# Performance work log

Hardware: AMD Instinct MI355X
Metric: run time of the kernel (lower is better)

## Reference

```python
import jax, jax.numpy as jnp
import numpy as np

EMB = 1024
HEADS = 16
HEAD_DIM = EMB // HEADS
FF = 4 * EMB


def _gelu_tanh(x):
    c = jnp.sqrt(jnp.asarray(2.0 / jnp.pi, x.dtype))
    return 0.5 * x * (1.0 + jnp.tanh(c * (x + 0.044715 * x ** 3)))


def _layernorm(x, scale, shift, eps=1e-5):
    mean = jnp.mean(x, axis=-1, keepdims=True)
    var = jnp.mean((x - mean) ** 2, axis=-1, keepdims=True)
    return scale * (x - mean) / jnp.sqrt(var + eps) + shift


def setup_inputs() -> dict:
    key = jax.random.key(0)
    ks = jax.random.split(key, 8)
    s = 0.02
    return {
        "x": jax.random.normal(ks[0], (2, 2048, EMB), jnp.float32),
        "w_q": jax.random.normal(ks[1], (EMB, EMB), jnp.float32) * s,
        "w_k": jax.random.normal(ks[2], (EMB, EMB), jnp.float32) * s,
        "w_v": jax.random.normal(ks[3], (EMB, EMB), jnp.float32) * s,
        "w_o": jax.random.normal(ks[4], (EMB, EMB), jnp.float32) * s,
        "b_o": jnp.zeros((EMB,), jnp.float32),
        "ln1_scale": jnp.ones((EMB,), jnp.float32),
        "ln1_shift": jnp.zeros((EMB,), jnp.float32),
        "ln2_scale": jnp.ones((EMB,), jnp.float32),
        "ln2_shift": jnp.zeros((EMB,), jnp.float32),
        "w_ff1": jax.random.normal(ks[5], (EMB, FF), jnp.float32) * s,
        "b_ff1": jnp.zeros((FF,), jnp.float32),
        "w_ff2": jax.random.normal(ks[6], (FF, EMB), jnp.float32) * s,
        "b_ff2": jnp.zeros((EMB,), jnp.float32),
    }


def _attention(x, w_q, w_k, w_v, w_o, b_o):
    b, n, _ = x.shape
    q = (x @ w_q).reshape(b, n, HEADS, HEAD_DIM).transpose(0, 2, 1, 3)  # bhnd
    k = (x @ w_k).reshape(b, n, HEADS, HEAD_DIM).transpose(0, 2, 1, 3)
    v = (x @ w_v).reshape(b, n, HEADS, HEAD_DIM).transpose(0, 2, 1, 3)
    scores = jnp.einsum("bhqd,bhkd->bhqk", q, k)
    causal = jnp.triu(jnp.ones((n, n), bool), k=1)
    scores = jnp.where(causal, -jnp.inf, scores)
    # original scales AFTER masking (-inf stays -inf)
    attn = jax.nn.softmax(scores / jnp.sqrt(jnp.asarray(HEAD_DIM, x.dtype)), axis=-1)
    ctx = jnp.einsum("bhqk,bhkd->bhqd", attn, v)
    ctx = ctx.transpose(0, 2, 1, 3).reshape(b, n, EMB)
    return ctx @ w_o + b_o


def reference(x, w_q, w_k, w_v, w_o, b_o, ln1_scale, ln1_shift,
              ln2_scale, ln2_shift, w_ff1, b_ff1, w_ff2, b_ff2):
    h = _layernorm(x, ln1_scale, ln1_shift)
    h = _attention(h, w_q, w_k, w_v, w_o, b_o)
    x = x + h  # dropout is identity at drop_rate=0 / eval
    h = _layernorm(x, ln2_scale, ln2_shift)
    h = _gelu_tanh(h @ w_ff1 + b_ff1) @ w_ff2 + b_ff2
    return x + h
```

## Files before the change

### kernel.cpp

```cpp
#include <hip/hip_runtime.h>
#include <math.h>

#define EMB 1024
#define HEADS 16
#define HD 64
#define FF_DIM 4096
#define SEQ 2048
#define BATCH 2
#define NTOK (BATCH * SEQ)

typedef __bf16 bf16x8 __attribute__((ext_vector_type(8)));
typedef float f32x4 __attribute__((ext_vector_type(4)));

__device__ __forceinline__ unsigned short f2bf(float f) {
    union { float f; unsigned int u; } v; v.f = f;
    unsigned int r = v.u + 0x7fff + ((v.u >> 16) & 1);
    return (unsigned short)(r >> 16);
}

__device__ __forceinline__ float gelu_f(float x) {
    const float A = 1.5957691216057308f;
    const float B = 0.07135481282989427f;
    float zz = x * (A + B * x * x);
    return x * __builtin_amdgcn_rcpf(1.f + __expf(-zz));
}

#define GLOAD_LDS16(g, l)                                                      \
    __builtin_amdgcn_global_load_lds(                                          \
        (const __attribute__((address_space(1))) void*)(g),                    \
        (__attribute__((address_space(3))) void*)(l), 16, 0, 0)

__global__ __launch_bounds__(256) void ln_kernel(const float* __restrict__ x,
                                                 const float* __restrict__ scale,
                                                 const float* __restrict__ shift,
                                                 unsigned short* __restrict__ out) {
    int row = blockIdx.x;
    const float* xr = x + (size_t)row * EMB;
    unsigned short* yr = out + (size_t)row * EMB;
    int t = threadIdx.x;

    float v[4];
    float s = 0.f, s2 = 0.f;
#pragma unroll
    for (int i = 0; i < 4; i++) {
        v[i] = xr[t + i * 256];
        s += v[i];
        s2 += v[i] * v[i];
    }
    for (int o = 32; o > 0; o >>= 1) {
        s += __shfl_down(s, o, 64);
        s2 += __shfl_down(s2, o, 64);
    }
    __shared__ float red[4], red2[4];
    int wave = t >> 6;
    if ((t & 63) == 0) { red[wave] = s; red2[wave] = s2; }
    __syncthreads();
    if (t == 0) {
        float a = 0.f, b = 0.f;
#pragma unroll
        for (int i = 0; i < 4; i++) { a += red[i]; b += red2[i]; }
        red[0] = a; red2[0] = b;
    }
    __syncthreads();
    float mean = red[0] * (1.f / EMB);
    float var = red2[0] * (1.f / EMB) - mean * mean;
    float rstd = rsqrtf(var + 1e-5f);
#pragma unroll
    for (int i = 0; i < 4; i++) {
        int c = t + i * 256;
        yr[c] = f2bf(scale[c] * (v[i] - mean) * rstd + shift[c]);
    }
}

__global__ __launch_bounds__(256) void transpose_cast6(
    const float* __restrict__ w0, const float* __restrict__ w1,
    const float* __restrict__ w2, const float* __restrict__ w3,
    const float* __restrict__ w4, const float* __restrict__ w5,
    unsigned short* __restrict__ o0, unsigned short* __restrict__ o1,
    unsigned short* __restrict__ o2, unsigned short* __restrict__ o3,
    unsigned short* __restrict__ o4, unsigned short* __restrict__ o5) {
    __shared__ float tile[64][65];
    int id = blockIdx.x;
    const float* src; unsigned short* dst; int K, N, lid;
    if (id < 256)       { src = w0; dst = o0; K = 1024; N = 1024; lid = id; }
    else if (id < 512)  { src = w1; dst = o1; K = 1024; N = 1024; lid = id - 256; }
    else if (id < 768)  { src = w2; dst = o2; K = 1024; N = 1024; lid = id - 512; }
    else if (id < 1024) { src = w3; dst = o3; K = 1024; N = 1024; lid = id - 768; }
    else if (id < 2048) { src = w4; dst = o4; K = 1024; N = 4096; lid = id - 1024; }
    else                { src = w5; dst = o5; K = 4096; N = 1024; lid = id - 2048; }
    int tn = N >> 6;
    int k0 = (lid / tn) << 6, n0 = (lid % tn) << 6;
    int t = threadIdx.x;
    int rr = t >> 6, cc = t & 63;
#pragma unroll
    for (int i = 0; i < 16; i++) {
        int r = i * 4 + rr;
        tile[r][cc] = src[(size_t)(k0 + r) * N + n0 + cc];
    }
    __syncthreads();
#pragma unroll
    for (int i = 0; i < 16; i++) {
        int r = i * 4 + rr;
        dst[(size_t)(n0 + r) * K + k0 + cc] = f2bf(tile[cc][r]);
    }
}

template <int EPI>
__global__ __launch_bounds__(256) void mfma_gemm(
    const unsigned short* __restrict__ A,
    const unsigned short* __restrict__ Bt,
    void* __restrict__ Cv,
    const float* __restrict__ bias,
    const float* __restrict__ resid,
    int M, int N, int K) {
    __shared__ unsigned short As[128 * 32];
    __shared__ unsigned short Bs[128 * 32];

    const int t = threadIdx.x;
    const int w = t >> 6, lane = t & 63;
    const int m0 = blockIdx.y * 128, n0 = blockIdx.x * 128;

    const int sr0 = (w << 5) + (lane >> 2);
    const int sr1 = sr0 + 16;
    const int p = lane & 3;
    const int c0 = p ^ ((sr0 >> 1) & 3);
    const int c1 = p ^ ((sr1 >> 1) & 3);
    const unsigned short* gA0 = A + (size_t)(m0 + sr0) * K + c0 * 8;
    const unsigned short* gA1 = A + (size_t)(m0 + sr1) * K + c1 * 8;
    const unsigned short* gB0 = Bt + (size_t)(n0 + sr0) * K + c0 * 8;
    const unsigned short* gB1 = Bt + (size_t)(n0 + sr1) * K + c1 * 8;
    unsigned short* lA0 = &As[(w << 5) * 32];
    unsigned short* lA1 = &As[((w << 5) + 16) * 32];
    unsigned short* lB0 = &Bs[(w << 5) * 32];
    unsigned short* lB1 = &Bs[((w << 5) + 16) * 32];

    const int mrow = (w >> 1) * 64, ncol = (w & 1) * 64;
    int aoff[4], boff[4];
#pragma unroll
    for (int i = 0; i < 4; i++) {
        int ra = mrow + i * 16 + (lane & 15);
        int pa = (lane >> 4) ^ ((ra >> 1) & 3);
        aoff[i] = ra * 32 + pa * 8;
        int rb = ncol + i * 16 + (lane & 15);
        int pb = (lane >> 4) ^ ((rb >> 1) & 3);
        boff[i] = rb * 32 + pb * 8;
    }

    f32x4 acc[4][4];
#pragma unroll
    for (int i = 0; i < 4; i++)
#pragma unroll
        for (int j = 0; j < 4; j++) acc[i][j] = (f32x4){0.f, 0.f, 0.f, 0.f};

    for (int k0 = 0; k0 < K; k0 += 32) {
        __syncthreads();
        GLOAD_LDS16(gA0, lA0);
        GLOAD_LDS16(gA1, lA1);
        GLOAD_LDS16(gB0, lB0);
        GLOAD_LDS16(gB1, lB1);
        gA0 += 32; gA1 += 32; gB0 += 32; gB1 += 32;
        __syncthreads();

        bf16x8 af[4], bfr[4];
#pragma unroll
        for (int i = 0; i < 4; i++) {
            af[i] = *reinterpret_cast<const bf16x8*>(&As[aoff[i]]);
            bfr[i] = *reinterpret_cast<const bf16x8*>(&Bs[boff[i]]);
        }
#pragma unroll
        for (int i = 0; i < 4; i++)
#pragma unroll
            for (int j = 0; j < 4; j++)
                acc[i][j] = __builtin_amdgcn_mfma_f32_16x16x32_bf16(
                    af[i], bfr[j], acc[i][j], 0, 0, 0);
    }

    const int ccol = lane & 15;
    const int crow = (lane >> 4) << 2;
#pragma unroll
    for (int i = 0; i < 4; i++) {
#pragma unroll
        for (int j = 0; j < 4; j++) {
            int col = n0 + ncol + j * 16 + ccol;
#pragma unroll
            for (int r = 0; r < 4; r++) {
                int row = m0 + mrow + i * 16 + crow + r;
                size_t idx = (size_t)row * N + col;
                float val = acc[i][j][r];
                ((unsigned short*)Cv)[idx] = f2bf(gelu_f(val + bias[col]));
            }
        }
    }
}

template <int EPI>
__global__ __launch_bounds__(256) void mfma_gemm64(
    const unsigned short* __restrict__ A,
    const unsigned short* __restrict__ Bt,
    float* __restrict__ C,
    const float* __restrict__ bias,
    const float* __restrict__ resid,
    int M, int N, int K) {
    __shared__ unsigned short As[128 * 32];
    __shared__ unsigned short Bs[64 * 32];

    const int t = threadIdx.x;
    const int w = t >> 6, lane = t & 63;
    const int m0 = blockIdx.y * 128, n0 = blockIdx.x * 64;

    const int sr0 = (w << 5) + (lane >> 2);
    const int sr1 = sr0 + 16;
    const int p = lane & 3;
    const int c0 = p ^ ((sr0 >> 1) & 3);
    const int c1 = p ^ ((sr1 >> 1) & 3);
    const unsigned short* gA0 = A + (size_t)(m0 + sr0) * K + c0 * 8;
    const unsigned short* gA1 = A + (size_t)(m0 + sr1) * K + c1 * 8;
    unsigned short* lA0 = &As[(w << 5) * 32];
    unsigned short* lA1 = &As[((w << 5) + 16) * 32];
    const int br = (w << 4) + (lane >> 2);
    const int cb = p ^ ((br >> 1) & 3);
    const unsigned short* gB0 = Bt + (size_t)(n0 + br) * K + cb * 8;
    unsigned short* lB0 = &Bs[(w << 4) * 32];

    int aoff[2], boff[4];
#pragma unroll
    for (int i = 0; i < 2; i++) {
        int ra = w * 32 + i * 16 + (lane & 15);
        int pa = (lane >> 4) ^ ((ra >> 1) & 3);
        aoff[i] = ra * 32 + pa * 8;
    }
#pragma unroll
    for (int j = 0; j < 4; j++) {
        int rb = j * 16 + (lane & 15);
        int pb = (lane >> 4) ^ ((rb >> 1) & 3);
        boff[j] = rb * 32 + pb * 8;
    }

    f32x4 acc[2][4];
#pragma unroll
    for (int i = 0; i < 2; i++)
#pragma unroll
        for (int j = 0; j < 4; j++) acc[i][j] = (f32x4){0.f, 0.f, 0.f, 0.f};

    for (int k0 = 0; k0 < K; k0 += 32) {
        __syncthreads();
        GLOAD_LDS16(gA0, lA0);
        GLOAD_LDS16(gA1, lA1);
        GLOAD_LDS16(gB0, lB0);
        gA0 += 32; gA1 += 32; gB0 += 32;
        __syncthreads();

        bf16x8 af[2], bfr[4];
#pragma unroll
        for (int i = 0; i < 2; i++)
            af[i] = *reinterpret_cast<const bf16x8*>(&As[aoff[i]]);
#pragma unroll
        for (int j = 0; j < 4; j++)
            bfr[j] = *reinterpret_cast<const bf16x8*>(&Bs[boff[j]]);
#pragma unroll
        for (int i = 0; i < 2; i++)
#pragma unroll
            for (int j = 0; j < 4; j++)
                acc[i][j] = __builtin_amdgcn_mfma_f32_16x16x32_bf16(
                    af[i], bfr[j], acc[i][j], 0, 0, 0);
    }

    const int ccol = lane & 15;
    const int crow = (lane >> 4) << 2;
#pragma unroll
    for (int i = 0; i < 2; i++) {
#pragma unroll
        for (int j = 0; j < 4; j++) {
            int col = n0 + j * 16 + ccol;
            float badd = bias[col];
#pragma unroll
            for (int r = 0; r < 4; r++) {
                int row = m0 + w * 32 + i * 16 + crow + r;
                size_t idx = (size_t)row * N + col;
                if constexpr (EPI == 1) {
                    C[idx] = acc[i][j][r] + badd + resid[idx];
                } else {
                    C[idx] = C[idx] + acc[i][j][r] + badd;
                }
            }
        }
    }
}

__global__ __launch_bounds__(256) void qkv_gemm(
    const unsigned short* __restrict__ lnO,
    const unsigned short* __restrict__ wqkT,
    const unsigned short* __restrict__ wvT,
    unsigned short* __restrict__ q,
    unsigned short* __restrict__ kb,
    unsigned short* __restrict__ vT) {
    __shared__ unsigned short As[128 * 32];
    __shared__ unsigned short Bs[128 * 32];

    const int t = threadIdx.x;
    const int w = t >> 6, lane = t & 63;
    const int bid = blockIdx.x;
    const bool qk = bid < 512;

    const unsigned short *A, *Bt;
    int m0, n0, N;
    if (qk) {
        A = lnO; Bt = wqkT;
        m0 = (bid >> 4) * 128; n0 = (bid & 15) * 128; N = 2048;
    } else {
        int lb = bid - 512;
        A = wvT; Bt = lnO;
        m0 = (lb & 7) * 128; n0 = (lb >> 3) * 128; N = 4096;
    }
    const int K = 1024;

    const int sr0 = (w << 5) + (lane >> 2);
    const int sr1 = sr0 + 16;
    const int p = lane & 3;
    const int c0 = p ^ ((sr0 >> 1) & 3);
    const int c1 = p ^ ((sr1 >> 1) & 3);
    const unsigned short* gA0 = A + (size_t)(m0 + sr0) * K + c0 * 8;
    const unsigned short* gA1 = A + (size_t)(m0 + sr1) * K + c1 * 8;
    const unsigned short* gB0 = Bt + (size_t)(n0 + sr0) * K + c0 * 8;
    const unsigned short* gB1 = Bt + (size_t)(n0 + sr1) * K + c1 * 8;
    unsigned short* lA0 = &As[(w << 5) * 32];
    unsigned short* lA1 = &As[((w << 5) + 16) * 32];
    unsigned short* lB0 = &Bs[(w << 5) * 32];
    unsigned short* lB1 = &Bs[((w << 5) + 16) * 32];

    const int mrow = (w >> 1) * 64, ncol = (w & 1) * 64;
    int aoff[4], boff[4];
#pragma unroll
    for (int i = 0; i < 4; i++) {
        int ra = mrow + i * 16 + (lane & 15);
        int pa = (lane >> 4) ^ ((ra >> 1) & 3);
        aoff[i] = ra * 32 + pa * 8;
        int rb = ncol + i * 16 + (lane & 15);
        int pb = (lane >> 4) ^ ((rb >> 1) & 3);
        boff[i] = rb * 32 + pb * 8;
    }

    f32x4 acc[4][4];
#pragma unroll
    for (int i = 0; i < 4; i++)
#pragma unroll
        for (int j = 0; j < 4; j++) acc[i][j] = (f32x4){0.f, 0.f, 0.f, 0.f};

    for (int k0 = 0; k0 < K; k0 += 32) {
        __syncthreads();
        GLOAD_LDS16(gA0, lA0);
        GLOAD_LDS16(gA1, lA1);
        GLOAD_LDS16(gB0, lB0);
        GLOAD_LDS16(gB1, lB1);
        gA0 += 32; gA1 += 32; gB0 += 32; gB1 += 32;
        __syncthreads();

        bf16x8 af[4], bfr[4];
#pragma unroll
        for (int i = 0; i < 4; i++) {
            af[i] = *reinterpret_cast<const bf16x8*>(&As[aoff[i]]);
            bfr[i] = *reinterpret_cast<const bf16x8*>(&Bs[boff[i]]);
        }
#pragma unroll
        for (int i = 0; i < 4; i++)
#pragma unroll
            for (int j = 0; j < 4; j++)
                acc[i][j] = __builtin_amdgcn_mfma_f32_16x16x32_bf16(
                    af[i], bfr[j], acc[i][j], 0, 0, 0);
    }

    const int ccol = lane & 15;
    const int crow = (lane >> 4) << 2;
    unsigned short* dst;
    int nbase;
    if (qk) {
        dst = (n0 < 1024) ? q : kb;
        nbase = n0 & 1023;
    } else {
        dst = vT;
        nbase = n0;
    }
    const int ldc = qk ? 1024 : 4096;
#pragma unroll
    for (int i = 0; i < 4; i++) {
#pragma unroll
        for (int j = 0; j < 4; j++) {
            int col = nbase + ncol + j * 16 + ccol;
#pragma unroll
            for (int r = 0; r < 4; r++) {
                int row = m0 + mrow + i * 16 + crow + r;
                dst[(size_t)row * ldc + col] = f2bf(acc[i][j][r]);
            }
        }
    }
}

__global__ __launch_bounds__(256) void attn_mfma(
    const unsigned short* __restrict__ Q,
    const unsigned short* __restrict__ K,
    const unsigned short* __restrict__ Vt,
    unsigned short* __restrict__ O) {
    __shared__ unsigned short Ks[2][64 * 64];
    __shared__ unsigned short Vs[2][64 * 64];
    __shared__ unsigned short Ps[4][16 * 64];

    const int t = threadIdx.x;
    const int w = t >> 6, lane = t & 63;
    const int l15 = lane & 15, l4 = lane >> 4;
    const int bh = blockIdx.y;
    const int b = bh >> 4, h = bh & 15;
    const int pair = blockIdx.x;

    const int sr = (w << 3) + (lane >> 3);
    const int sc = lane & 7;
    const int c = sc ^ (sr & 7);
    const unsigned short* kbase = K + ((size_t)(b * SEQ)) * EMB + h * HD;
    const unsigned short* vbase = Vt + ((size_t)(h * HD)) * (size_t)NTOK + (size_t)b * SEQ;
    unsigned short* Pw = &Ps[w][0];

#define STAGE(k0s, buf)                                                        \
    do {                                                                       \
        GLOAD_LDS16(kbase + (size_t)((k0s) + sr) * EMB + c * 8,                \
                    &Ks[buf][(w << 3) * 64]);                                  \
        GLOAD_LDS16(kbase + (size_t)((k0s) + sr + 32) * EMB + c * 8,           \
                    &Ks[buf][((w << 3) + 32) * 64]);                           \
        GLOAD_LDS16(vbase + (size_t)sr * NTOK + (k0s) + c * 8,                 \
                    &Vs[buf][(w << 3) * 64]);                                  \
        GLOAD_LDS16(vbase + (size_t)(sr + 32) * NTOK + (k0s) + c * 8,          \
                    &Vs[buf][((w << 3) + 32) * 64]);                           \
    } while (0)

    const float C1 = 0.125f * 1.4426950408889634f;
    const float C2 = 3.0f * 1.4426950408889634f;

#pragma unroll
    for (int phase = 0; phase < 2; phase++) {
        const int qt = phase ? pair : (31 - pair);
        const int q0 = qt * 64;

        const unsigned short* qg =
            Q + ((size_t)(b * SEQ + q0 + w * 16 + l15)) * EMB + h * HD + l4 * 8;
        bf16x8 qf0 = *(const bf16x8*)qg;
        bf16x8 qf1 = *(const bf16x8*)(qg + 32);
        const int qrow_c = q0 + w * 16 + l4 * 4;

        float lsum[4] = {0.f, 0.f, 0.f, 0.f};
        f32x4 Oacc[4];
#pragma unroll
        for (int j = 0; j < 4; j++) Oacc[j] = (f32x4){0.f, 0.f, 0.f, 0.f};

        const int ntiles = qt + 1;
        __syncthreads();
        STAGE(0, 0);
        for (int tile = 0; tile < ntiles; tile++) {
            const int k0 = tile * 64;
            const int buf = tile & 1;
            __syncthreads();
            if (tile + 1 < ntiles) STAGE(k0 + 64, buf ^ 1);

            f32x4 S[4];
#pragma unroll
            for (int j = 0; j < 4; j++) S[j] = (f32x4){0.f, 0.f, 0.f, 0.f};
#pragma unroll
            for (int s = 0; s < 2; s++) {
                bf16x8 qf = s ? qf1 : qf0;
#pragma unroll
                for (int j = 0; j < 4; j++) {
                    int rk = 16 * j + l15;
                    int phys = (s * 4 + l4) ^ (rk & 7);
                    bf16x8 kf = *(const bf16x8*)&Ks[buf][rk * 64 + phys * 8];
                    S[j] = __builtin_amdgcn_mfma_f32_16x16x32_bf16(qf, kf, S[j], 0, 0, 0);
                }
            }

            if (tile == ntiles - 1) {
#pragma unroll
                for (int j = 0; j < 4; j++)
#pragma unroll
                    for (int r = 0; r < 4; r++) {
                        float e = exp2f(S[j][r] * C1 - C2);
                        if (k0 + 16 * j + l15 > qrow_c + r) e = 0.f;
                        S[j][r] = e;
                        lsum[r] += e;
                    }
            } else {
#pragma unroll
                for (int j = 0; j < 4; j++)
#pragma unroll
                    for (int r = 0; r < 4; r++) {
                        float e = exp2f(S[j][r] * C1 - C2);
                        S[j][r] = e;
                        lsum[r] += e;
                    }
            }

#pragma unroll
            for (int r = 0; r < 4; r++) {
                int row = l4 * 4 + r;
#pragma unroll
                for (int j = 0; j < 4; j++) {
                    int col = 16 * j + l15;
                    int phys = (col >> 3) ^ (row & 7);
                    Pw[row * 64 + phys * 8 + (col & 7)] = f2bf(S[j][r]);
                }
            }

#pragma unroll
            for (int s = 0; s < 2; s++) {
                int pphys = (s * 4 + l4) ^ (l15 & 7);
                bf16x8 pf = *(const bf16x8*)&Pw[l15 * 64 + pphys * 8];
#pragma unroll
                for (int j = 0; j < 4; j++) {
                    int rv = 16 * j + l15;
                    int vphys = (s * 4 + l4) ^ (rv & 7);
                    bf16x8 vf = *(const bf16x8*)&Vs[buf][rv * 64 + vphys * 8];
                    Oacc[j] = __builtin_amdgcn_mfma_f32_16x16x32_bf16(pf, vf, Oacc[j], 0, 0, 0);
                }
            }
        }

#pragma unroll
        for (int r = 0; r < 4; r++) {
            float l = lsum[r];
#pragma unroll
            for (int off = 1; off < 16; off <<= 1)
                l += __shfl_xor(l, off, 64);
            float inv = 1.f / l;
            size_t rowb = (size_t)(b * SEQ + qrow_c + r) * EMB + h * HD;
#pragma unroll
            for (int j = 0; j < 4; j++)
                O[rowb + 16 * j + l15] = f2bf(Oacc[j][r] * inv);
        }
    }
#undef STAGE
}

extern "C" void kernel_launch(void* const* d_in, const int* in_sizes, int n_in,
                              void* d_out, int out_size, void* d_ws, size_t ws_size,
                              hipStream_t stream) {
    const float* x     = (const float*)d_in[0];
    const float* w_q   = (const float*)d_in[1];
    const float* w_k   = (const float*)d_in[2];
    const float* w_v   = (const float*)d_in[3];
    const float* w_o   = (const float*)d_in[4];
    const float* b_o   = (const float*)d_in[5];
    const float* ln1s  = (const float*)d_in[6];
    const float* ln1b  = (const float*)d_in[7];
    const float* ln2s  = (const float*)d_in[8];
    const float* ln2b  = (const float*)d_in[9];
    const float* w_ff1 = (const float*)d_in[10];
    const float* b_ff1 = (const float*)d_in[11];
    const float* w_ff2 = (const float*)d_in[12];
    const float* b_ff2 = (const float*)d_in[13];
    float* out = (float*)d_out;

    char* p = (char*)d_ws;
    unsigned short* lnO  = (unsigned short*)p; p += (size_t)NTOK * EMB * 2;
    unsigned short* q    = (unsigned short*)p; p += (size_t)NTOK * EMB * 2;
    unsigned short* kbuf = (unsigned short*)p; p += (size_t)NTOK * EMB * 2;
    unsigned short* vT   = (unsigned short*)p; p += (size_t)NTOK * EMB * 2;
    unsigned short* ctx  = (unsigned short*)p; p += (size_t)NTOK * EMB * 2;
    unsigned short* ff1a = (unsigned short*)p; p += (size_t)NTOK * FF_DIM * 2;
    unsigned short* wqkT = (unsigned short*)p; p += (size_t)2 * EMB * EMB * 2;
    unsigned short* wvT  = (unsigned short*)p; p += (size_t)EMB * EMB * 2;
    unsigned short* woT  = (unsigned short*)p; p += (size_t)EMB * EMB * 2;
    unsigned short* wf1T = (unsigned short*)p; p += (size_t)FF_DIM * EMB * 2;
    unsigned short* wf2T = (unsigned short*)p; p += (size_t)EMB * FF_DIM * 2;

    dim3 blk(256);
    dim3 gN64(EMB / 64, NTOK / 128);
    dim3 gFF1(FF_DIM / 128, NTOK / 128);
    dim3 gAttn(16, BATCH * HEADS);

    transpose_cast6<<<3072, blk, 0, stream>>>(
        w_q, w_k, w_v, w_o, w_ff1, w_ff2,
        wqkT, wqkT + (size_t)EMB * EMB, wvT, woT, wf1T, wf2T);
    ln_kernel<<<NTOK, blk, 0, stream>>>(x, ln1s, ln1b, lnO);
    qkv_gemm<<<768, blk, 0, stream>>>(lnO, wqkT, wvT, q, kbuf, vT);
    attn_mfma<<<gAttn, blk, 0, stream>>>(q, kbuf, vT, ctx);
    mfma_gemm64<1><<<gN64, blk, 0, stream>>>(ctx, woT, out, b_o, x, NTOK, EMB, EMB);
    ln_kernel<<<NTOK, blk, 0, stream>>>(out, ln2s, ln2b, ctx);
    mfma_gemm<2><<<gFF1, blk, 0, stream>>>(ctx, wf1T, ff1a, b_ff1, nullptr, NTOK, FF_DIM, EMB);
    mfma_gemm64<3><<<gN64, blk, 0, stream>>>(ff1a, wf2T, out, b_ff2, nullptr, NTOK, EMB, FF_DIM);
}
```

Baseline: 377.1 us.

## Double-buffer LDS in GEMM kernels and reorder block rasterization along M

Adds ping-pong LDS buffers to the FF1, 64-wide and QKV GEMMs so the next K-slice's global-to-LDS load is issued before computing on the current one, leaving one barrier per iteration instead of two. Grid and block-index mapping are also swapped so consecutive blocks walk the M dimension while sharing a weight tile, which changes L2 reuse. The FF1 GEMM is de-templated and its bias load hoisted out of the inner loop. LDS use per block doubles, which may reduce occupancy, and correctness depends on the async LDS loads finishing before the next barrier.

Measured after the change: 372.5 us. No clear change (-1.2%).

```diff
diff --git a/kernel.cpp b/kernel.cpp
--- a/kernel.cpp
+++ b/kernel.cpp
@@ -105,20 +105,18 @@
     }
 }
 
-template <int EPI>
-__global__ __launch_bounds__(256) void mfma_gemm(
+__global__ __launch_bounds__(256) void ff1_gemm(
     const unsigned short* __restrict__ A,
     const unsigned short* __restrict__ Bt,
-    void* __restrict__ Cv,
+    unsigned short* __restrict__ C,
     const float* __restrict__ bias,
-    const float* __restrict__ resid,
     int M, int N, int K) {
-    __shared__ unsigned short As[128 * 32];
-    __shared__ unsigned short Bs[128 * 32];
+    __shared__ unsigned short As[2][128 * 32];
+    __shared__ unsigned short Bs[2][128 * 32];
 
     const int t = threadIdx.x;
     const int w = t >> 6, lane = t & 63;
-    const int m0 = blockIdx.y * 128, n0 = blockIdx.x * 128;
+    const int m0 = blockIdx.x * 128, n0 = blockIdx.y * 128;
 
     const int sr0 = (w << 5) + (lane >> 2);
     const int sr1 = sr0 + 16;
@@ -129,10 +127,7 @@
     const unsigned short* gA1 = A + (size_t)(m0 + sr1) * K + c1 * 8;
     const unsigned short* gB0 = Bt + (size_t)(n0 + sr0) * K + c0 * 8;
     const unsigned short* gB1 = Bt + (size_t)(n0 + sr1) * K + c1 * 8;
-    unsigned short* lA0 = &As[(w << 5) * 32];
-    unsigned short* lA1 = &As[((w << 5) + 16) * 32];
-    unsigned short* lB0 = &Bs[(w << 5) * 32];
-    unsigned short* lB1 = &Bs[((w << 5) + 16) * 32];
+    const int lo0 = (w << 5) * 32, lo1 = ((w << 5) + 16) * 32;
 
     const int mrow = (w >> 1) * 64, ncol = (w & 1) * 64;
     int aoff[4], boff[4];
@@ -152,20 +147,27 @@
 #pragma unroll
         for (int j = 0; j < 4; j++) acc[i][j] = (f32x4){0.f, 0.f, 0.f, 0.f};
 
-    for (int k0 = 0; k0 < K; k0 += 32) {
+#define STG1(b)                                                                \
+    do {                                                                       \
+        GLOAD_LDS16(gA0, &As[b][lo0]);                                         \
+        GLOAD_LDS16(gA1, &As[b][lo1]);                                         \
+        GLOAD_LDS16(gB0, &Bs[b][lo0]);                                         \
+        GLOAD_LDS16(gB1, &Bs[b][lo1]);                                         \
+        gA0 += 32; gA1 += 32; gB0 += 32; gB1 += 32;                            \
+    } while (0)
+
+    STG1(0);
+    const int nk = K >> 5;
+    for (int it = 0; it < nk; it++) {
+        const int buf = it & 1;
         __syncthreads();
-        GLOAD_LDS16(gA0, lA0);
-        GLOAD_LDS16(gA1, lA1);
-        GLOAD_LDS16(gB0, lB0);
-        GLOAD_LDS16(gB1, lB1);
-        gA0 += 32; gA1 += 32; gB0 += 32; gB1 += 32;
-        __syncthreads();
+        if (it + 1 < nk) STG1(buf ^ 1);
 
         bf16x8 af[4], bfr[4];
 #pragma unroll
         for (int i = 0; i < 4; i++) {
-            af[i] = *reinterpret_cast<const bf16x8*>(&As[aoff[i]]);
-            bfr[i] = *reinterpret_cast<const bf16x8*>(&Bs[boff[i]]);
+            af[i] = *reinterpret_cast<const bf16x8*>(&As[buf][aoff[i]]);
+            bfr[i] = *reinterpret_cast<const bf16x8*>(&Bs[buf][boff[i]]);
         }
 #pragma unroll
         for (int i = 0; i < 4; i++)
@@ -174,6 +176,7 @@
                 acc[i][j] = __builtin_amdgcn_mfma_f32_16x16x32_bf16(
                     af[i], bfr[j], acc[i][j], 0, 0, 0);
     }
+#undef STG1
 
     const int ccol = lane & 15;
     const int crow = (lane >> 4) << 2;
@@ -182,12 +185,11 @@
 #pragma unroll
         for (int j = 0; j < 4; j++) {
             int col = n0 + ncol + j * 16 + ccol;
+            float badd = bias[col];
 #pragma unroll
             for (int r = 0; r < 4; r++) {
                 int row = m0 + mrow + i * 16 + crow + r;
-                size_t idx = (size_t)row * N + col;
-                float val = acc[i][j][r];
-                ((unsigned short*)Cv)[idx] = f2bf(gelu_f(val + bias[col]));
+                C[(size_t)row * N + col] = f2bf(gelu_f(acc[i][j][r] + badd));
             }
         }
     }
@@ -201,12 +203,12 @@
     const float* __restrict__ bias,
     const float* __restrict__ resid,
     int M, int N, int K) {
-    __shared__ unsigned short As[128 * 32];
-    __shared__ unsigned short Bs[64 * 32];
+    __shared__ unsigned short As[2][128 * 32];
+    __shared__ unsigned short Bs[2][64 * 32];
 
     const int t = threadIdx.x;
     const int w = t >> 6, lane = t & 63;
-    const int m0 = blockIdx.y * 128, n0 = blockIdx.x * 64;
+    const int m0 = blockIdx.x * 128, n0 = blockIdx.y * 64;
 
     const int sr0 = (w << 5) + (lane >> 2);
     const int sr1 = sr0 + 16;
@@ -215,12 +217,11 @@
     const int c1 = p ^ ((sr1 >> 1) & 3);
     const unsigned short* gA0 = A + (size_t)(m0 + sr0) * K + c0 * 8;
     const unsigned short* gA1 = A + (size_t)(m0 + sr1) * K + c1 * 8;
-    unsigned short* lA0 = &As[(w << 5) * 32];
-    unsigned short* lA1 = &As[((w << 5) + 16) * 32];
     const int br = (w << 4) + (lane >> 2);
     const int cb = p ^ ((br >> 1) & 3);
     const unsigned short* gB0 = Bt + (size_t)(n0 + br) * K + cb * 8;
-    unsigned short* lB0 = &Bs[(w << 4) * 32];
+    const int lao0 = (w << 5) * 32, lao1 = ((w << 5) + 16) * 32;
+    const int lbo = (w << 4) * 32;
 
     int aoff[2], boff[4];
 #pragma unroll
@@ -242,21 +243,28 @@
 #pragma unroll
         for (int j = 0; j < 4; j++) acc[i][j] = (f32x4){0.f, 0.f, 0.f, 0.f};
 
-    for (int k0 = 0; k0 < K; k0 += 32) {
+#define STG64(b)                                                               \
+    do {                                                                       \
+        GLOAD_LDS16(gA0, &As[b][lao0]);                                        \
+        GLOAD_LDS16(gA1, &As[b][lao1]);                                        \
+        GLOAD_LDS16(gB0, &Bs[b][lbo]);                                         \
+        gA0 += 32; gA1 += 32; gB0 += 32;                                       \
+    } while (0)
+
+    STG64(0);
+    const int nk = K >> 5;
+    for (int it = 0; it < nk; it++) {
+        const int buf = it & 1;
         __syncthreads();
-        GLOAD_LDS16(gA0, lA0);
-        GLOAD_LDS16(gA1, lA1);
-        GLOAD_LDS16(gB0, lB0);
-        gA0 += 32; gA1 += 32; gB0 += 32;
-        __syncthreads();
+        if (it + 1 < nk) STG64(buf ^ 1);
 
         bf16x8 af[2], bfr[4];
 #pragma unroll
         for (int i = 0; i < 2; i++)
-            af[i] = *reinterpret_cast<const bf16x8*>(&As[aoff[i]]);
+            af[i] = *reinterpret_cast<const bf16x8*>(&As[buf][aoff[i]]);
 #pragma unroll
         for (int j = 0; j < 4; j++)
-            bfr[j] = *reinterpret_cast<const bf16x8*>(&Bs[boff[j]]);
+            bfr[j] = *reinterpret_cast<const bf16x8*>(&Bs[buf][boff[j]]);
 #pragma unroll
         for (int i = 0; i < 2; i++)
 #pragma unroll
@@ -264,6 +272,7 @@
                 acc[i][j] = __builtin_amdgcn_mfma_f32_16x16x32_bf16(
                     af[i], bfr[j], acc[i][j], 0, 0, 0);
     }
+#undef STG64
 
     const int ccol = lane & 15;
     const int crow = (lane >> 4) << 2;
@@ -294,8 +303,8 @@
     unsigned short* __restrict__ q,
     unsigned short* __restrict__ kb,
     unsigned short* __restrict__ vT) {
-    __shared__ unsigned short As[128 * 32];
-    __shared__ unsigned short Bs[128 * 32];
+    __shared__ unsigned short As[2][128 * 32];
+    __shared__ unsigned short Bs[2][128 * 32];
 
     const int t = threadIdx.x;
     const int w = t >> 6, lane = t & 63;
@@ -306,7 +315,7 @@
     int m0, n0, N;
     if (qk) {
         A = lnO; Bt = wqkT;
-        m0 = (bid >> 4) * 128; n0 = (bid & 15) * 128; N = 2048;
+        m0 = (bid & 31) * 128; n0 = (bid >> 5) * 128; N = 2048;
     } else {
         int lb = bid - 512;
         A = wvT; Bt = lnO;
@@ -323,10 +332,7 @@
     const unsigned short* gA1 = A + (size_t)(m0 + sr1) * K + c1 * 8;
     const unsigned short* gB0 = Bt + (size_t)(n0 + sr0) * K + c0 * 8;
     const unsigned short* gB1 = Bt + (size_t)(n0 + sr1) * K + c1 * 8;
-    unsigned short* lA0 = &As[(w << 5) * 32];
-    unsigned short* lA1 = &As[((w << 5) + 16) * 32];
-    unsigned short* lB0 = &Bs[(w << 5) * 32];
-    unsigned short* lB1 = &Bs[((w << 5) + 16) * 32];
+    const int lo0 = (w << 5) * 32, lo1 = ((w << 5) + 16) * 32;
 
     const int mrow = (w >> 1) * 64, ncol = (w & 1) * 64;
     int aoff[4], boff[4];
@@ -346,20 +352,27 @@
 #pragma unroll
         for (int j = 0; j < 4; j++) acc[i][j] = (f32x4){0.f, 0.f, 0.f, 0.f};
 
-    for (int k0 = 0; k0 < K; k0 += 32) {
+#define STGQ(b)                                                                \
+    do {                                                                       \
+        GLOAD_LDS16(gA0, &As[b][lo0]);                                         \
+        GLOAD_LDS16(gA1, &As[b][lo1]);                                         \
+        GLOAD_LDS16(gB0, &Bs[b][lo0]);                                         \
+        GLOAD_LDS16(gB1, &Bs[b][lo1]);                                         \
+        gA0 += 32; gA1 += 32; gB0 += 32; gB1 += 32;                            \
+    } while (0)
+
+    STGQ(0);
+    const int nk = K >> 5;
+    for (int it = 0; it < nk; it++) {
+        const int buf = it & 1;
         __syncthreads();
-        GLOAD_LDS16(gA0, lA0);
-        GLOAD_LDS16(gA1, lA1);
-        GLOAD_LDS16(gB0, lB0);
-        GLOAD_LDS16(gB1, lB1);
-        gA0 += 32; gA1 += 32; gB0 += 32; gB1 += 32;
-        __syncthreads();
+        if (it + 1 < nk) STGQ(buf ^ 1);
 
         bf16x8 af[4], bfr[4];
 #pragma unroll
         for (int i = 0; i < 4; i++) {
-            af[i] = *reinterpret_cast<const bf16x8*>(&As[aoff[i]]);
-            bfr[i] = *reinterpret_cast<const bf16x8*>(&Bs[boff[i]]);
+            af[i] = *reinterpret_cast<const bf16x8*>(&As[buf][aoff[i]]);
+            bfr[i] = *reinterpret_cast<const bf16x8*>(&Bs[buf][boff[i]]);
         }
 #pragma unroll
         for (int i = 0; i < 4; i++)
@@ -368,6 +381,7 @@
                 acc[i][j] = __builtin_amdgcn_mfma_f32_16x16x32_bf16(
                     af[i], bfr[j], acc[i][j], 0, 0, 0);
     }
+#undef STGQ
 
     const int ccol = lane & 15;
     const int crow = (lane >> 4) << 2;
@@ -568,8 +582,8 @@
     unsigned short* wf2T = (unsigned short*)p; p += (size_t)EMB * FF_DIM * 2;
 
     dim3 blk(256);
-    dim3 gN64(EMB / 64, NTOK / 128);
-    dim3 gFF1(FF_DIM / 128, NTOK / 128);
+    dim3 gN64(NTOK / 128, EMB / 64);
+    dim3 gFF1(NTOK / 128, FF_DIM / 128);
     dim3 gAttn(16, BATCH * HEADS);
 
     transpose_cast6<<<3072, blk, 0, stream>>>(
@@ -580,6 +594,6 @@
     attn_mfma<<<gAttn, blk, 0, stream>>>(q, kbuf, vT, ctx);
     mfma_gemm64<1><<<gN64, blk, 0, stream>>>(ctx, woT, out, b_o, x, NTOK, EMB, EMB);
     ln_kernel<<<NTOK, blk, 0, stream>>>(out, ln2s, ln2b, ctx);
-    mfma_gemm<2><<<gFF1, blk, 0, stream>>>(ctx, wf1T, ff1a, b_ff1, nullptr, NTOK, FF_DIM, EMB);
+    ff1_gemm<<<gFF1, blk, 0, stream>>>(ctx, wf1T, ff1a, b_ff1, NTOK, FF_DIM, EMB);
     mfma_gemm64<3><<<gN64, blk, 0, stream>>>(ff1a, wf2T, out, b_ff2, nullptr, NTOK, EMB, FF_DIM);
 }
```
